# Optimization experiments

Measured on AMD Instinct MI355X. Metric: run time of the kernel, lower is better.

Reference implementation:

```python
import jax, jax.numpy as jnp
import numpy as np

N_TEST, N_TRAIN, D = 16384, 8192, 64


def setup_inputs() -> dict:
    key = jax.random.key(0)
    k1, k2, k3 = jax.random.split(key, 3)
    test_X = jax.random.normal(k1, (N_TEST, D), dtype=jnp.float32)
    train_X = jax.random.normal(k2, (N_TRAIN, D), dtype=jnp.float32)
    alphas = jax.random.normal(k3, (N_TRAIN, 1), dtype=jnp.float32)
    lengthscale = jnp.ones((1,), dtype=jnp.float32)
    return {"test_X": test_X, "train_X": train_X, "alphas": alphas, "lengthscale": lengthscale}


def reference(test_X, train_X, alphas, lengthscale):
    # gpytorch RBFKernel: scale inputs by lengthscale, squared dist, exp(-0.5 * d2)
    xs = test_X / lengthscale    # [n_test, d]
    ts = train_X / lengthscale   # [n_train, d]
    sq = (jnp.sum(xs * xs, axis=-1, keepdims=True)
          - 2.0 * (xs @ ts.T)
          + jnp.sum(ts * ts, axis=-1)[None, :])  # [n_test, n_train]
    K = jnp.exp(-0.5 * jnp.maximum(sq, 0.0))
    return K @ alphas  # [n_test, 1]
```

## Files before the change

### kernel.cpp

```cpp
#include <hip/hip_runtime.h>

#define NTEST  16384
#define NTRAIN 8192
#define DIM    64
#define NCOLSPLIT 16
#define WPB    8

typedef _Float16 f16x8  __attribute__((ext_vector_type(8)));
typedef float    f32x16 __attribute__((ext_vector_type(16)));

#define LOG2E 1.4426950408889634f

#define GLOAD_LDS16(gsrc, ldst)                                                     \
    __builtin_amdgcn_global_load_lds(                                               \
        (const __attribute__((address_space(1))) unsigned int*)(gsrc),              \
        (__attribute__((address_space(3))) unsigned int*)(ldst), 16, 0, 0)

__global__ __launch_bounds__(256) void krr_prep(
    const float* __restrict__ test_X, const float* __restrict__ train_X,
    const float* __restrict__ alphas, const float* __restrict__ lengthscale,
    _Float16* __restrict__ A_hi, _Float16* __restrict__ B_hi,
    float* __restrict__ nx2, float* __restrict__ wt, float* __restrict__ out)
{
    int gwave = (blockIdx.x * 256 + threadIdx.x) >> 6;
    int lane  = threadIdx.x & 63;
    bool is_test = gwave < NTEST;
    int row = is_test ? gwave : gwave - NTEST;
    const float* src = is_test ? test_X : train_X;

    float ls   = lengthscale[0];
    float inv2 = 1.0f / (ls * ls);
    float s1   = inv2 * LOG2E;
    float cn   = -0.5f * inv2 * LOG2E;

    float x = src[(size_t)row * DIM + lane];

    if (is_test) {
        A_hi[(size_t)row * DIM + lane] = (_Float16)(x * s1);
    } else {
        _Float16 h = (_Float16)x;
        int t  = row >> 5, lr = row & 31;
        int kk = lane >> 4, hi = (lane >> 3) & 1, e = lane & 7;
        size_t dst = (size_t)t * 2048 + (size_t)kk * 512 + (size_t)(hi * 32 + lr) * 8 + e;
        B_hi[dst] = h;
    }

    float s = x * x;
    s += __shfl_xor(s, 1);  s += __shfl_xor(s, 2);  s += __shfl_xor(s, 4);
    s += __shfl_xor(s, 8);  s += __shfl_xor(s, 16); s += __shfl_xor(s, 32);
    if (lane == 0) {
        if (is_test) { nx2[row] = s * cn; out[row] = 0.0f; }
        else         wt[row]  = alphas[row] * __builtin_amdgcn_exp2f(cn * s);
    }
}

__global__ __launch_bounds__(512) void krr_mfma(
    const _Float16* __restrict__ A_hi, const _Float16* __restrict__ B_hi,
    const float* __restrict__ nx2, const float* __restrict__ wt,
    const float* __restrict__ lengthscale, float* __restrict__ out)
{
    alignas(16) __shared__ _Float16 BsA[8 * 2048];
    alignas(16) __shared__ _Float16 BsB[8 * 2048];
    __shared__ float wts[512];

    const int tid   = threadIdx.x;
    const int lane  = tid & 63;
    const int wave  = tid >> 6;
    const int rbase = blockIdx.x * 256 + wave * 32;
    const int cb    = blockIdx.y;

    #define STAGE8(p, buf)                                                      \
        {                                                                       \
            const _Float16* gt = B_hi + ((size_t)cb * 16 + (p) * 8 + wave) * 2048 \
                               + (size_t)lane * 8;                              \
            _Float16* lt0 = (buf) + (size_t)wave * 2048;                        \
            GLOAD_LDS16(gt,        lt0);                                        \
            GLOAD_LDS16(gt + 512,  lt0 + 512);                                  \
            GLOAD_LDS16(gt + 1024, lt0 + 1024);                                 \
            GLOAD_LDS16(gt + 1536, lt0 + 1536);                                 \
        }

    #define COMPUTE8(p, buf)                                                    \
        {                                                                       \
            const _Float16* pbase = (buf) + (size_t)lane * 8;                   \
            f16x8 bhA[4], bhB[4];                                               \
            _Pragma("unroll")                                                   \
            for (int kk = 0; kk < 4; ++kk) {                                    \
                bhA[kk] = *reinterpret_cast<const f16x8*>(pbase + kk * 512);    \
                bhB[kk] = *reinterpret_cast<const f16x8*>(pbase + 2048 + kk * 512); \
            }                                                                   \
            _Pragma("unroll 1")                                                 \
            for (int lt = 0; lt < 8; lt += 2) {                                 \
                f32x16 CA = __builtin_amdgcn_mfma_f32_32x32x16_f16(ah[0], bhA[0], nxcv, 0, 0, 0); \
                f32x16 CB = __builtin_amdgcn_mfma_f32_32x32x16_f16(ah[0], bhB[0], nxcv, 0, 0, 0); \
                _Pragma("unroll")                                               \
                for (int kk = 1; kk < 4; ++kk) {                                \
                    CA = __builtin_amdgcn_mfma_f32_32x32x16_f16(ah[kk], bhA[kk], CA, 0, 0, 0); \
                    CB = __builtin_amdgcn_mfma_f32_32x32x16_f16(ah[kk], bhB[kk], CB, 0, 0, 0); \
                }                                                               \
                const int wtb = ((p) * 8 + lt) * 32 + (lane & 31);              \
                const float wA = wts[wtb];                                      \
                const float wB = wts[wtb + 32];                                 \
                if (lt < 6) {                                                   \
                    const _Float16* pn = pbase + (size_t)(lt + 2) * 2048;       \
                    _Pragma("unroll")                                           \
                    for (int kk = 0; kk < 4; ++kk) {                            \
                        bhA[kk] = *reinterpret_cast<const f16x8*>(pn + kk * 512); \
                        bhB[kk] = *reinterpret_cast<const f16x8*>(pn + 2048 + kk * 512); \
                    }                                                           \
                }                                                               \
                _Pragma("unroll")                                               \
                for (int r = 0; r < 16; ++r) {                                  \
                    acc[r] = fmaf(__builtin_amdgcn_exp2f(CA[r]), wA, acc[r]);   \
                    acc[r] = fmaf(__builtin_amdgcn_exp2f(CB[r]), wB, acc[r]);   \
                }                                                               \
            }                                                                   \
        }

    STAGE8(0, BsA);
    wts[tid] = wt[cb * 512 + tid];

    const int arow = rbase + (lane & 31);
    const int koff = (lane >> 5) * 8;

    f16x8 ah[4];
    #pragma unroll
    for (int kk = 0; kk < 4; ++kk)
        ah[kk] = *reinterpret_cast<const f16x8*>(A_hi + (size_t)arow * DIM + kk * 16 + koff);

    f32x16 nxcv;
    #pragma unroll
    for (int r = 0; r < 16; ++r) {
        int row = (r & 3) + 8 * (r >> 2) + 4 * (lane >> 5);
        nxcv[r] = nx2[rbase + row];
    }

    float acc[16];
    #pragma unroll
    for (int r = 0; r < 16; ++r) acc[r] = 0.0f;

    __syncthreads();

    STAGE8(1, BsB);
    COMPUTE8(0, BsA);

    __syncthreads();

    COMPUTE8(1, BsB);

    #undef STAGE8
    #undef COMPUTE8

    #pragma unroll
    for (int r = 0; r < 16; ++r) {
        float v = acc[r];
        v += __shfl_xor(v, 1);  v += __shfl_xor(v, 2);  v += __shfl_xor(v, 4);
        v += __shfl_xor(v, 8);  v += __shfl_xor(v, 16);
        if ((lane & 31) == 0) {
            int row = (r & 3) + 8 * (r >> 2) + 4 * (lane >> 5);
            atomicAdd(&out[rbase + row], v);
        }
    }
}

#define TCHUNK 512
#define NCHUNK (NTRAIN / TCHUNK)
__global__ __launch_bounds__(256, 4) void krr_main(
    const float* __restrict__ test_X, const float* __restrict__ train_X,
    const float* __restrict__ alphas, const float* __restrict__ lengthscale,
    float* __restrict__ out)
{
    __shared__ float nt_lds[TCHUNK];
    __shared__ float al_lds[TCHUNK];
    const int tid = threadIdx.x;
    const int i   = blockIdx.x * 256 + tid;
    const int j0  = blockIdx.y * TCHUNK;
    const float ls   = lengthscale[0];
    const float inv2 = 1.0f / (ls * ls);
    for (int jj = tid; jj < TCHUNK; jj += 256) {
        const float4* tr = reinterpret_cast<const float4*>(train_X + (size_t)(j0 + jj) * DIM);
        float s = 0.f;
        #pragma unroll
        for (int k = 0; k < DIM / 4; ++k) {
            float4 t = tr[k];
            s += t.x * t.x + t.y * t.y + t.z * t.z + t.w * t.w;
        }
        nt_lds[jj] = s * inv2;
        al_lds[jj] = alphas[j0 + jj];
    }
    __syncthreads();
    float xr[DIM]; float nxv = 0.f;
    {
        const float4* xp = reinterpret_cast<const float4*>(test_X + (size_t)i * DIM);
        #pragma unroll
        for (int k = 0; k < DIM / 4; ++k) {
            float4 v = xp[k];
            xr[4*k+0] = v.x; xr[4*k+1] = v.y; xr[4*k+2] = v.z; xr[4*k+3] = v.w;
            nxv += v.x*v.x + v.y*v.y + v.z*v.z + v.w*v.w;
        }
        nxv *= inv2;
        #pragma unroll
        for (int k = 0; k < DIM; ++k) xr[k] *= inv2;
    }
    float acc = 0.f;
    for (int jj = 0; jj < TCHUNK; ++jj) {
        const float* trow = train_X + (size_t)(j0 + jj) * DIM;
        float d0 = 0.f, d1 = 0.f, d2 = 0.f, d3 = 0.f;
        #pragma unroll
        for (int k4 = 0; k4 < DIM / 4; ++k4) {
            float4 t = reinterpret_cast<const float4*>(trow)[k4];
            d0 = fmaf(xr[4*k4+0], t.x, d0);
            d1 = fmaf(xr[4*k4+1], t.y, d1);
            d2 = fmaf(xr[4*k4+2], t.z, d2);
            d3 = fmaf(xr[4*k4+3], t.w, d3);
        }
        float dot = (d0 + d1) + (d2 + d3);
        float sq  = nxv + nt_lds[jj] - 2.0f * dot;
        sq = fmaxf(sq, 0.0f);
        acc = fmaf(__expf(-0.5f * sq), al_lds[jj], acc);
    }
    atomicAdd(&out[i], acc);
}

extern "C" void kernel_launch(void* const* d_in, const int* in_sizes, int n_in,
                              void* d_out, int out_size, void* d_ws, size_t ws_size,
                              hipStream_t stream) {
    const float* test_X      = (const float*)d_in[0];
    const float* train_X     = (const float*)d_in[1];
    const float* alphas      = (const float*)d_in[2];
    const float* lengthscale = (const float*)d_in[3];
    float* out = (float*)d_out;

    const size_t need = (size_t)(NTEST + NTRAIN) * DIM * sizeof(_Float16)
                      + (NTEST + NTRAIN) * sizeof(float);
    if (ws_size >= need) {
        _Float16* A_hi = (_Float16*)d_ws;
        _Float16* B_hi = A_hi + (size_t)NTEST * DIM;
        float*    nx2  = (float*)(B_hi + (size_t)NTRAIN * DIM);
        float*    wtp  = nx2 + NTEST;

        krr_prep<<<(NTEST + NTRAIN) / 4, 256, 0, stream>>>(
            test_X, train_X, alphas, lengthscale, A_hi, B_hi, nx2, wtp, out);

        dim3 grid(NTEST / 256, NCOLSPLIT);
        krr_mfma<<<grid, 64 * WPB, 0, stream>>>(A_hi, B_hi, nx2, wtp,
                                                lengthscale, out);
    } else {
        hipMemsetAsync(out, 0, NTEST * sizeof(float), stream);
        dim3 grid(NTEST / 256, NCHUNK);
        krr_main<<<grid, 256, 0, stream>>>(test_X, train_X, alphas, lengthscale, out);
    }
}
```

Baseline: 38.84 us.

## Give each wave two 32-row test tiles sharing B fragments, halve block size

Restructures the MFMA kernel so each of 4 waves handles 64 test rows (two 32-row A tiles) and reuses every LDS-loaded train fragment for both, instead of 8 waves each doing 32 rows over two train tiles. This halves LDS reads of B per MFMA and lowers block size to 256 threads, while each wave now issues twice the staging loads. It costs more registers (two A fragment sets, two accumulators) and fewer waves per block for latency hiding.

```diff
diff --git a/kernel.cpp b/kernel.cpp
--- a/kernel.cpp
+++ b/kernel.cpp
@@ -4,7 +4,7 @@
 #define NTRAIN 8192
 #define DIM    64
 #define NCOLSPLIT 16
-#define WPB    8
+#define WPB    4
 
 typedef _Float16 f16x8  __attribute__((ext_vector_type(8)));
 typedef float    f32x16 __attribute__((ext_vector_type(16)));
@@ -54,7 +54,7 @@
     }
 }
 
-__global__ __launch_bounds__(512) void krr_mfma(
+__global__ __launch_bounds__(256, 1) void krr_mfma(
     const _Float16* __restrict__ A_hi, const _Float16* __restrict__ B_hi,
     const float* __restrict__ nx2, const float* __restrict__ wt,
     const float* __restrict__ lengthscale, float* __restrict__ out)
@@ -66,78 +66,81 @@
     const int tid   = threadIdx.x;
     const int lane  = tid & 63;
     const int wave  = tid >> 6;
-    const int rbase = blockIdx.x * 256 + wave * 32;
+    const int rbase = blockIdx.x * 256 + wave * 64;
     const int cb    = blockIdx.y;
 
     #define STAGE8(p, buf)                                                      \
         {                                                                       \
-            const _Float16* gt = B_hi + ((size_t)cb * 16 + (p) * 8 + wave) * 2048 \
+            const _Float16* g0 = B_hi + ((size_t)cb * 16 + (p) * 8 + wave * 2) * 2048 \
                                + (size_t)lane * 8;                              \
-            _Float16* lt0 = (buf) + (size_t)wave * 2048;                        \
-            GLOAD_LDS16(gt,        lt0);                                        \
-            GLOAD_LDS16(gt + 512,  lt0 + 512);                                  \
-            GLOAD_LDS16(gt + 1024, lt0 + 1024);                                 \
-            GLOAD_LDS16(gt + 1536, lt0 + 1536);                                 \
+            _Float16* l0 = (buf) + (size_t)(wave * 2) * 2048;                   \
+            GLOAD_LDS16(g0,        l0);                                         \
+            GLOAD_LDS16(g0 + 512,  l0 + 512);                                   \
+            GLOAD_LDS16(g0 + 1024, l0 + 1024);                                  \
+            GLOAD_LDS16(g0 + 1536, l0 + 1536);                                  \
+            GLOAD_LDS16(g0 + 2048, l0 + 2048);                                  \
+            GLOAD_LDS16(g0 + 2560, l0 + 2560);                                  \
+            GLOAD_LDS16(g0 + 3072, l0 + 3072);                                  \
+            GLOAD_LDS16(g0 + 3584, l0 + 3584);                                  \
         }
 
     #define COMPUTE8(p, buf)                                                    \
         {                                                                       \
             const _Float16* pbase = (buf) + (size_t)lane * 8;                   \
-            f16x8 bhA[4], bhB[4];                                               \
+            f16x8 bh[4];                                                        \
             _Pragma("unroll")                                                   \
-            for (int kk = 0; kk < 4; ++kk) {                                    \
-                bhA[kk] = *reinterpret_cast<const f16x8*>(pbase + kk * 512);    \
-                bhB[kk] = *reinterpret_cast<const f16x8*>(pbase + 2048 + kk * 512); \
-            }                                                                   \
+            for (int kk = 0; kk < 4; ++kk)                                      \
+                bh[kk] = *reinterpret_cast<const f16x8*>(pbase + kk * 512);     \
             _Pragma("unroll 1")                                                 \
-            for (int lt = 0; lt < 8; lt += 2) {                                 \
-                f32x16 CA = __builtin_amdgcn_mfma_f32_32x32x16_f16(ah[0], bhA[0], nxcv, 0, 0, 0); \
-                f32x16 CB = __builtin_amdgcn_mfma_f32_32x32x16_f16(ah[0], bhB[0], nxcv, 0, 0, 0); \
+            for (int lt = 0; lt < 8; ++lt) {                                    \
+                f32x16 C1 = __builtin_amdgcn_mfma_f32_32x32x16_f16(ah1[0], bh[0], nxcv1, 0, 0, 0); \
+                f32x16 C2 = __builtin_amdgcn_mfma_f32_32x32x16_f16(ah2[0], bh[0], nxcv2, 0, 0, 0); \
                 _Pragma("unroll")                                               \
                 for (int kk = 1; kk < 4; ++kk) {                                \
-                    CA = __builtin_amdgcn_mfma_f32_32x32x16_f16(ah[kk], bhA[kk], CA, 0, 0, 0); \
-                    CB = __builtin_amdgcn_mfma_f32_32x32x16_f16(ah[kk], bhB[kk], CB, 0, 0, 0); \
+                    C1 = __builtin_amdgcn_mfma_f32_32x32x16_f16(ah1[kk], bh[kk], C1, 0, 0, 0); \
+                    C2 = __builtin_amdgcn_mfma_f32_32x32x16_f16(ah2[kk], bh[kk], C2, 0, 0, 0); \
                 }                                                               \
-                const int wtb = ((p) * 8 + lt) * 32 + (lane & 31);              \
-                const float wA = wts[wtb];                                      \
-                const float wB = wts[wtb + 32];                                 \
-                if (lt < 6) {                                                   \
-                    const _Float16* pn = pbase + (size_t)(lt + 2) * 2048;       \
+                const float w = wts[((p) * 8 + lt) * 32 + (lane & 31)];         \
+                if (lt < 7) {                                                   \
+                    const _Float16* pn = pbase + (size_t)(lt + 1) * 2048;       \
                     _Pragma("unroll")                                           \
-                    for (int kk = 0; kk < 4; ++kk) {                            \
-                        bhA[kk] = *reinterpret_cast<const f16x8*>(pn + kk * 512); \
-                        bhB[kk] = *reinterpret_cast<const f16x8*>(pn + 2048 + kk * 512); \
-                    }                                                           \
+                    for (int kk = 0; kk < 4; ++kk)                              \
+                        bh[kk] = *reinterpret_cast<const f16x8*>(pn + kk * 512); \
                 }                                                               \
                 _Pragma("unroll")                                               \
                 for (int r = 0; r < 16; ++r) {                                  \
-                    acc[r] = fmaf(__builtin_amdgcn_exp2f(CA[r]), wA, acc[r]);   \
-                    acc[r] = fmaf(__builtin_amdgcn_exp2f(CB[r]), wB, acc[r]);   \
+                    acc1[r] = fmaf(__builtin_amdgcn_exp2f(C1[r]), w, acc1[r]);  \
+                    acc2[r] = fmaf(__builtin_amdgcn_exp2f(C2[r]), w, acc2[r]);  \
                 }                                                               \
             }                                                                   \
         }
 
     STAGE8(0, BsA);
-    wts[tid] = wt[cb * 512 + tid];
-
-    const int arow = rbase + (lane & 31);
-    const int koff = (lane >> 5) * 8;
-
-    f16x8 ah[4];
-    #pragma unroll
-    for (int kk = 0; kk < 4; ++kk)
-        ah[kk] = *reinterpret_cast<const f16x8*>(A_hi + (size_t)arow * DIM + kk * 16 + koff);
-
-    f32x16 nxcv;
+    wts[tid]       = wt[cb * 512 + tid];
+    wts[tid + 256] = wt[cb * 512 + tid + 256];
+
+    const int arow1 = rbase + (lane & 31);
+    const int arow2 = arow1 + 32;
+    const int koff  = (lane >> 5) * 8;
+
+    f16x8 ah1[4], ah2[4];
+    #pragma unroll
+    for (int kk = 0; kk < 4; ++kk) {
+        ah1[kk] = *reinterpret_cast<const f16x8*>(A_hi + (size_t)arow1 * DIM + kk * 16 + koff);
+        ah2[kk] = *reinterpret_cast<const f16x8*>(A_hi + (size_t)arow2 * DIM + kk * 16 + koff);
+    }
+
+    f32x16 nxcv1, nxcv2;
     #pragma unroll
     for (int r = 0; r < 16; ++r) {
         int row = (r & 3) + 8 * (r >> 2) + 4 * (lane >> 5);
-        nxcv[r] = nx2[rbase + row];
-    }
-
-    float acc[16];
-    #pragma unroll
-    for (int r = 0; r < 16; ++r) acc[r] = 0.0f;
+        nxcv1[r] = nx2[rbase + row];
+        nxcv2[r] = nx2[rbase + 32 + row];
+    }
+
+    float acc1[16], acc2[16];
+    #pragma unroll
+    for (int r = 0; r < 16; ++r) { acc1[r] = 0.0f; acc2[r] = 0.0f; }
 
     __syncthreads();
 
@@ -153,12 +156,22 @@
 
     #pragma unroll
     for (int r = 0; r < 16; ++r) {
-        float v = acc[r];
+        float v = acc1[r];
         v += __shfl_xor(v, 1);  v += __shfl_xor(v, 2);  v += __shfl_xor(v, 4);
         v += __shfl_xor(v, 8);  v += __shfl_xor(v, 16);
         if ((lane & 31) == 0) {
             int row = (r & 3) + 8 * (r >> 2) + 4 * (lane >> 5);
             atomicAdd(&out[rbase + row], v);
+        }
+    }
+    #pragma unroll
+    for (int r = 0; r < 16; ++r) {
+        float v = acc2[r];
+        v += __shfl_xor(v, 1);  v += __shfl_xor(v, 2);  v += __shfl_xor(v, 4);
+        v += __shfl_xor(v, 8);  v += __shfl_xor(v, 16);
+        if ((lane & 31) == 0) {
+            int row = (r & 3) + 8 * (r >> 2) + 4 * (lane >> 5);
+            atomicAdd(&out[rbase + 32 + row], v);
         }
     }
 }
```

Result: slower. 45.04 us (+16.0%).

## Shrink LDS staging to 4-tile double buffers and raise occupancy hint

Applied to the files above, without the earlier changes.

Cuts each shared-memory staging buffer from 8 train tiles to 4 and runs four smaller double-buffered stages instead of two. The compute loop now handles one tile per iteration instead of two interleaved tiles with register prefetch. A min-blocks-per-CU hint of 6 is added to launch_bounds. The aim is to lower LDS and register use so more blocks can be resident, at the cost of more barriers and less instruction-level parallelism between MFMA and exp work.

```diff
diff --git a/kernel.cpp b/kernel.cpp
--- a/kernel.cpp
+++ b/kernel.cpp
@@ -54,13 +54,13 @@
     }
 }
 
-__global__ __launch_bounds__(512) void krr_mfma(
+__global__ __launch_bounds__(512, 6) void krr_mfma(
     const _Float16* __restrict__ A_hi, const _Float16* __restrict__ B_hi,
     const float* __restrict__ nx2, const float* __restrict__ wt,
     const float* __restrict__ lengthscale, float* __restrict__ out)
 {
-    alignas(16) __shared__ _Float16 BsA[8 * 2048];
-    alignas(16) __shared__ _Float16 BsB[8 * 2048];
+    alignas(16) __shared__ _Float16 BsA[4 * 2048];
+    alignas(16) __shared__ _Float16 BsB[4 * 2048];
     __shared__ float wts[512];
 
     const int tid   = threadIdx.x;
@@ -69,55 +69,36 @@
     const int rbase = blockIdx.x * 256 + wave * 32;
     const int cb    = blockIdx.y;
 
-    #define STAGE8(p, buf)                                                      \
+    #define STAGE4(u, buf)                                                      \
         {                                                                       \
-            const _Float16* gt = B_hi + ((size_t)cb * 16 + (p) * 8 + wave) * 2048 \
-                               + (size_t)lane * 8;                              \
-            _Float16* lt0 = (buf) + (size_t)wave * 2048;                        \
-            GLOAD_LDS16(gt,        lt0);                                        \
-            GLOAD_LDS16(gt + 512,  lt0 + 512);                                  \
-            GLOAD_LDS16(gt + 1024, lt0 + 1024);                                 \
-            GLOAD_LDS16(gt + 1536, lt0 + 1536);                                 \
-        }
-
-    #define COMPUTE8(p, buf)                                                    \
+            const _Float16* g = B_hi + ((size_t)cb * 16 + (u) * 4) * 2048       \
+                              + (size_t)wave * 1024 + (size_t)lane * 8;         \
+            _Float16* l = (buf) + (size_t)wave * 1024;                          \
+            GLOAD_LDS16(g,       l);                                            \
+            GLOAD_LDS16(g + 512, l + 512);                                      \
+        }
+
+    #define COMPUTE4(p, buf)                                                    \
         {                                                                       \
-            const _Float16* pbase = (buf) + (size_t)lane * 8;                   \
-            f16x8 bhA[4], bhB[4];                                               \
-            _Pragma("unroll")                                                   \
-            for (int kk = 0; kk < 4; ++kk) {                                    \
-                bhA[kk] = *reinterpret_cast<const f16x8*>(pbase + kk * 512);    \
-                bhB[kk] = *reinterpret_cast<const f16x8*>(pbase + 2048 + kk * 512); \
+            _Pragma("unroll 1")                                                 \
+            for (int lt = 0; lt < 4; ++lt) {                                    \
+                const _Float16* pt = (buf) + (size_t)lt * 2048 + (size_t)lane * 8; \
+                f16x8 bh[4];                                                    \
+                _Pragma("unroll")                                               \
+                for (int kk = 0; kk < 4; ++kk)                                  \
+                    bh[kk] = *reinterpret_cast<const f16x8*>(pt + kk * 512);    \
+                f32x16 C = __builtin_amdgcn_mfma_f32_32x32x16_f16(ah[0], bh[0], nxcv, 0, 0, 0); \
+                _Pragma("unroll")                                               \
+                for (int kk = 1; kk < 4; ++kk)                                  \
+                    C = __builtin_amdgcn_mfma_f32_32x32x16_f16(ah[kk], bh[kk], C, 0, 0, 0); \
+                const float w = wts[((p) * 4 + lt) * 32 + (lane & 31)];         \
+                _Pragma("unroll")                                               \
+                for (int r = 0; r < 16; ++r)                                    \
+                    acc[r] = fmaf(__builtin_amdgcn_exp2f(C[r]), w, acc[r]);     \
             }                                                                   \
-            _Pragma("unroll 1")                                                 \
-            for (int lt = 0; lt < 8; lt += 2) {                                 \
-                f32x16 CA = __builtin_amdgcn_mfma_f32_32x32x16_f16(ah[0], bhA[0], nxcv, 0, 0, 0); \
-                f32x16 CB = __builtin_amdgcn_mfma_f32_32x32x16_f16(ah[0], bhB[0], nxcv, 0, 0, 0); \
-                _Pragma("unroll")                                               \
-                for (int kk = 1; kk < 4; ++kk) {                                \
-                    CA = __builtin_amdgcn_mfma_f32_32x32x16_f16(ah[kk], bhA[kk], CA, 0, 0, 0); \
-                    CB = __builtin_amdgcn_mfma_f32_32x32x16_f16(ah[kk], bhB[kk], CB, 0, 0, 0); \
-                }                                                               \
-                const int wtb = ((p) * 8 + lt) * 32 + (lane & 31);              \
-                const float wA = wts[wtb];                                      \
-                const float wB = wts[wtb + 32];                                 \
-                if (lt < 6) {                                                   \
-                    const _Float16* pn = pbase + (size_t)(lt + 2) * 2048;       \
-                    _Pragma("unroll")                                           \
-                    for (int kk = 0; kk < 4; ++kk) {                            \
-                        bhA[kk] = *reinterpret_cast<const f16x8*>(pn + kk * 512); \
-                        bhB[kk] = *reinterpret_cast<const f16x8*>(pn + 2048 + kk * 512); \
-                    }                                                           \
-                }                                                               \
-                _Pragma("unroll")                                               \
-                for (int r = 0; r < 16; ++r) {                                  \
-                    acc[r] = fmaf(__builtin_amdgcn_exp2f(CA[r]), wA, acc[r]);   \
-                    acc[r] = fmaf(__builtin_amdgcn_exp2f(CB[r]), wB, acc[r]);   \
-                }                                                               \
-            }                                                                   \
-        }
-
-    STAGE8(0, BsA);
+        }
+
+    STAGE4(0, BsA);
     wts[tid] = wt[cb * 512 + tid];
 
     const int arow = rbase + (lane & 31);
@@ -141,15 +122,22 @@
 
     __syncthreads();
 
-    STAGE8(1, BsB);
-    COMPUTE8(0, BsA);
-
-    __syncthreads();
-
-    COMPUTE8(1, BsB);
-
-    #undef STAGE8
-    #undef COMPUTE8
+    STAGE4(1, BsB);
+    COMPUTE4(0, BsA);
+    __syncthreads();
+
+    STAGE4(2, BsA);
+    COMPUTE4(1, BsB);
+    __syncthreads();
+
+    STAGE4(3, BsB);
+    COMPUTE4(2, BsA);
+    __syncthreads();
+
+    COMPUTE4(3, BsB);
+
+    #undef STAGE4
+    #undef COMPUTE4
 
     #pragma unroll
     for (int r = 0; r < 16; ++r) {
```

Measured after the change: 37.30 us. 1.04x faster.
